# Kernel tuning notes

Hardware: AMD Instinct MI355X
Metric: run time of the kernel (lower is better)

The kernel has to match this reference:

```python
import jax, jax.numpy as jnp
from jax import lax
import numpy as np

V, E, H = 32000, 256, 256  # vocab, embed_dim, rnn_cell_size
B, S = 64, 2048


def setup_inputs() -> dict:
    key = jax.random.key(0)
    ks = jax.random.split(key, 8)
    inv_sqrt_h = 1.0 / np.sqrt(H)
    return {
        "text_inputs": jax.random.randint(ks[0], (B, S), 0, V),
        "mask_input": jnp.ones((B, S), jnp.float32),
        "len_seq": jax.random.randint(ks[1], (B,), 1, S),
        "embed": jax.random.normal(ks[2], (V, E), jnp.float32) * 0.1,
        "W_ih": jax.random.uniform(ks[3], (4 * H, E), jnp.float32, -inv_sqrt_h, inv_sqrt_h),
        "W_hh": jax.random.uniform(ks[4], (4 * H, H), jnp.float32, -inv_sqrt_h, inv_sqrt_h),
        "b_ih": jax.random.uniform(ks[5], (4 * H,), jnp.float32, -inv_sqrt_h, inv_sqrt_h),
        "b_hh": jax.random.uniform(ks[6], (4 * H,), jnp.float32, -inv_sqrt_h, inv_sqrt_h),
    }


def _lstm(x_bse, W_ih, W_hh, b_ih, b_hh):
    # Precompute input contribution in one big GEMM: [B,S,4H]
    pre = jnp.einsum('bse,ge->bsg', x_bse, W_ih) + b_ih
    pre = pre.transpose(1, 0, 2)  # [S,B,4H] for scan over time
    b = x_bse.shape[0]
    h0 = jnp.zeros((b, H), x_bse.dtype)

    def step(carry, p_t):
        h, c = carry
        gates = p_t + h @ W_hh.T + b_hh  # [B,4H], PyTorch gate order i,f,g,o
        i, f, g, o = jnp.split(gates, 4, axis=-1)
        c = jax.nn.sigmoid(f) * c + jax.nn.sigmoid(i) * jnp.tanh(g)
        h = jax.nn.sigmoid(o) * jnp.tanh(c)
        return (h, c), h

    _, hs = lax.scan(step, (h0, h0), pre)  # hs: [S,B,H]
    return hs.transpose(1, 0, 2)  # [B,S,H]


def reference(text_inputs, mask_input, len_seq, embed, W_ih, W_hh, b_ih, b_hh):
    # embedded_dropout with dropout=0 -> plain embedding lookup
    x = embed[text_inputs]  # [B,S,E]
    # sort by length descending (module sorts but never packs)
    order = jnp.argsort(-len_seq)
    x_sorted = x[order]
    out = _lstm(x_sorted, W_ih, W_hh, b_ih, b_hh)
    # LockedDropout inactive in eval -> identity
    inv = jnp.argsort(order)
    out = out[inv]
    return out * mask_input[..., None]
```

## Files before the change

kernel.cpp:

```cpp
#include <hip/hip_runtime.h>

#define S_LEN 2048

typedef _Float16 f16;
typedef _Float16 f16x8 __attribute__((ext_vector_type(8)));
typedef float f32x4 __attribute__((ext_vector_type(4)));

__device__ __forceinline__ float sigf(float x) {
  x = fminf(fmaxf(x, -30.f), 30.f);
  float e = __builtin_amdgcn_exp2f(-1.44269504089f * x);
  return __builtin_amdgcn_rcpf(1.f + e);
}
__device__ __forceinline__ float tanh_fast(float x) {
  x = fminf(fmaxf(x, -15.f), 15.f);
  float e = __builtin_amdgcn_exp2f(2.88539008178f * x);
  return 1.f - 2.f * __builtin_amdgcn_rcpf(e + 1.f);
}

__device__ __forceinline__ void st_hx(unsigned* p, unsigned v) {
  __hip_atomic_store(p, v, __ATOMIC_RELAXED, __HIP_MEMORY_SCOPE_AGENT);
}
__device__ __forceinline__ unsigned ld_hx(const unsigned* p) {
  return __hip_atomic_load(p, __ATOMIC_RELAXED, __HIP_MEMORY_SCOPE_AGENT);
}
__device__ __forceinline__ float swz8(float v) {
  int i = __builtin_bit_cast(int, v);
  int r = __builtin_amdgcn_ds_swizzle(i, 0x201F);
  return __builtin_bit_cast(float, r);
}

__global__ void convert_k(const float* __restrict__ Wih, const float* __restrict__ Whh,
                          const float* __restrict__ bih, const float* __restrict__ bhh,
                          f16* __restrict__ W16, float* __restrict__ bias,
                          unsigned* __restrict__ hx) {
  int i = blockIdx.x * blockDim.x + threadIdx.x;
  int n = i >> 9, k = i & 511;
  W16[i] = (f16)((k < 256) ? Whh[n * 256 + k] : Wih[n * 256 + (k - 256)]);
  if (i < 1024) bias[i] = bih[i] + bhh[i];
  if (i < 32768) hx[i] = 0u;
}

__global__ __launch_bounds__(256, 1) void lstm_k(
    const f16* __restrict__ W16, const float* __restrict__ bias,
    const int* __restrict__ text, const float* __restrict__ embed,
    const float* __restrict__ mask, float* __restrict__ out,
    unsigned* __restrict__ hx) {
  __shared__ __align__(16) f16 h_sw[2][16 * 256];
  __shared__ __align__(16) f16 x_sw[4][16 * 256];

  const int tid = threadIdx.x;
  const int g = blockIdx.x & 7;
  const int slice = blockIdx.x >> 3;
  const int b0 = g * 8;
  const int j0 = slice * 32;

  const int wv = tid >> 6;
  const int l = tid & 63;
  const int kg = l >> 4;
  const int c16 = l & 15;
  const int asw = (c16 & 7) << 3;
  const int gsel = c16 >> 3;
  const int jloc = wv * 8 + (c16 & 7);
  const int jg = j0 + jloc;

  const int r = tid >> 5;
  const int jl = tid & 31;
  const int rsw = (r & 7) << 3;
  const int pd = jl * 8;

  {
    f16x8 z = {(f16)0.f, (f16)0.f, (f16)0.f, (f16)0.f,
               (f16)0.f, (f16)0.f, (f16)0.f, (f16)0.f};
    *(f16x8*)&h_sw[0][tid * 16] = z;
    *(f16x8*)&h_sw[0][tid * 16 + 8] = z;
    *(f16x8*)&h_sw[1][tid * 16] = z;
    *(f16x8*)&h_sw[1][tid * 16 + 8] = z;
  }

  const float bi = bias[0 * 256 + jg];
  const float bf = bias[1 * 256 + jg];
  const float bg = bias[2 * 256 + jg];
  const float bo = bias[3 * 256 + jg];

  f16x8 barr0[16], barr1[16];
  {
    const f16* w0 = W16 + (size_t)(gsel * 256 + jg) * 512 + kg * 8;
    const f16* w1 = W16 + (size_t)((2 + gsel) * 256 + jg) * 512 + kg * 8;
#pragma unroll
    for (int kc = 0; kc < 16; kc++) {
      barr0[kc] = *(const f16x8*)(w0 + kc * 32);
      barr1[kc] = *(const f16x8*)(w1 + kc * 32);
    }
  }

  const int upd = (kg < 2);
  const int bA = kg * 4 + gsel * 2;
  const int bB = bA + 1;
  const int bAc = upd ? bA : 0;
  const int bBc = upd ? bB : 0;
  float ccA = 0.f, ccB = 0.f;

  const size_t trow = (size_t)(b0 + r) * S_LEN;
#pragma unroll 1
  for (int pf = 0; pf < 4; pf++) {
    int idx = text[trow + pf];
    const float4* ep = (const float4*)(embed + (size_t)idx * 256 + pd);
    float4 v0 = ep[0], v1 = ep[1];
    f16x8 hv = {(f16)v0.x, (f16)v0.y, (f16)v0.z, (f16)v0.w,
                (f16)v1.x, (f16)v1.y, (f16)v1.z, (f16)v1.w};
    *(f16x8*)&x_sw[pf][(r * 256 + pd) ^ rsw] = hv;
  }
  float4 rxa, rxb;
  int idx_r;
  {
    int idx4 = text[trow + 4];
    const float4* ep = (const float4*)(embed + (size_t)idx4 * 256 + pd);
    rxa = ep[0];
    rxb = ep[1];
    idx_r = text[trow + 5];
  }

  int offs[7];
#pragma unroll
  for (int p = 0; p < 7; p++) {
    int ps = p + (p >= slice);
    offs[p] = (g * 8 + ps) * 256 + r * 32 + jl;
  }
  const int own_off = (g * 8 + slice) * 256 + bAc * 32 + jloc;

  float mA = mask[(size_t)(b0 + bAc) * S_LEN];
  float mB = mask[(size_t)(b0 + bBc) * S_LEN];

  __syncthreads();

  f32x4 xacc0 = {0.f, 0.f, 0.f, 0.f}, xacc1 = {0.f, 0.f, 0.f, 0.f};
#pragma unroll
  for (int kc = 0; kc < 8; kc++) {
    f16x8 a = *(const f16x8*)&x_sw[0][(c16 * 256 + kc * 32 + kg * 8) ^ asw];
    xacc0 = __builtin_amdgcn_mfma_f32_16x16x32_f16(a, barr0[8 + kc], xacc0, 0, 0, 0);
    xacc1 = __builtin_amdgcn_mfma_f32_16x16x32_f16(a, barr1[8 + kc], xacc1, 0, 0, 0);
  }

  for (int t = 0; t < S_LEN; t++) {
    const f16* hs = h_sw[t & 1];
    f32x4 acc0 = xacc0, acc1 = xacc1;
#pragma unroll
    for (int kc = 0; kc < 8; kc++) {
      f16x8 a = *(const f16x8*)&hs[(c16 * 256 + kc * 32 + kg * 8) ^ asw];
      acc0 = __builtin_amdgcn_mfma_f32_16x16x32_f16(a, barr0[kc], acc0, 0, 0, 0);
      acc1 = __builtin_amdgcn_mfma_f32_16x16x32_f16(a, barr1[kc], acc1, 0, 0, 0);
    }

    float o0_0 = swz8(acc0[0]), o0_1 = swz8(acc0[1]), o0_2 = swz8(acc0[2]), o0_3 = swz8(acc0[3]);
    float o1_0 = swz8(acc1[0]), o1_1 = swz8(acc1[1]), o1_2 = swz8(acc1[2]), o1_3 = swz8(acc1[3]);

    float a0A = gsel ? acc0[2] : acc0[0], a1A = gsel ? acc1[2] : acc1[0];
    float x0A = gsel ? o0_2 : o0_0, x1A = gsel ? o1_2 : o1_0;
    float a0B = gsel ? acc0[3] : acc0[1], a1B = gsel ? acc1[3] : acc1[1];
    float x0B = gsel ? o0_3 : o0_1, x1B = gsel ? o1_3 : o1_1;

    float giA = (gsel ? x0A : a0A) + bi, gfA = (gsel ? a0A : x0A) + bf;
    float ggA = (gsel ? x1A : a1A) + bg, goA = (gsel ? a1A : x1A) + bo;
    float giB = (gsel ? x0B : a0B) + bi, gfB = (gsel ? a0B : x0B) + bf;
    float ggB = (gsel ? x1B : a1B) + bg, goB = (gsel ? a1B : x1B) + bo;

    ccA = sigf(gfA) * ccA + sigf(giA) * tanh_fast(ggA);
    float hA = sigf(goA) * tanh_fast(ccA);
    ccB = sigf(gfB) * ccB + sigf(giB) * tanh_fast(ggB);
    float hB = sigf(goB) * tanh_fast(ccB);

    const int par = (t + 1) & 1;
    unsigned* hb = hx + par * 16384;
    f16* hd = h_sw[par];

    if (upd) {
      unsigned wA = ((unsigned)(t + 1) << 16) |
                    (unsigned)__builtin_bit_cast(unsigned short, (f16)hA);
      unsigned wB = ((unsigned)(t + 1) << 16) |
                    (unsigned)__builtin_bit_cast(unsigned short, (f16)hB);
      st_hx(hb + own_off, wA);
      st_hx(hb + own_off + 32, wB);
      out[((size_t)(b0 + bA) * S_LEN + t) * 256 + jg] = hA * mA;
      out[((size_t)(b0 + bB) * S_LEN + t) * 256 + jg] = hB * mB;
      hd[(bA * 256 + jg) ^ ((bA & 7) << 3)] = (f16)hA;
      hd[(bB * 256 + jg) ^ ((bB & 7) << 3)] = (f16)hB;
    }

    if (t + 1 < S_LEN) {
      mA = mask[(size_t)(b0 + bAc) * S_LEN + (t + 1)];
      mB = mask[(size_t)(b0 + bBc) * S_LEN + (t + 1)];

      const f16* xs = x_sw[(t + 1) & 3];
      f32x4 nx0 = {0.f, 0.f, 0.f, 0.f}, nx1 = {0.f, 0.f, 0.f, 0.f};
#pragma unroll
      for (int kc = 0; kc < 8; kc++) {
        f16x8 a = *(const f16x8*)&xs[(c16 * 256 + kc * 32 + kg * 8) ^ asw];
        nx0 = __builtin_amdgcn_mfma_f32_16x16x32_f16(a, barr0[8 + kc], nx0, 0, 0, 0);
        nx1 = __builtin_amdgcn_mfma_f32_16x16x32_f16(a, barr1[8 + kc], nx1, 0, 0, 0);
      }
      xacc0 = nx0;
      xacc1 = nx1;

      if (t + 4 < S_LEN) {
        f16x8 hv = {(f16)rxa.x, (f16)rxa.y, (f16)rxa.z, (f16)rxa.w,
                    (f16)rxb.x, (f16)rxb.y, (f16)rxb.z, (f16)rxb.w};
        *(f16x8*)&x_sw[t & 3][(r * 256 + pd) ^ rsw] = hv;
      }
      if (t + 5 < S_LEN) {
        const float4* ep = (const float4*)(embed + (size_t)idx_r * 256 + pd);
        rxa = ep[0];
        rxb = ep[1];
      }
      if (t + 6 < S_LEN) idx_r = text[trow + t + 6];

      const unsigned expv = (unsigned)(t + 1);
      unsigned need = 0x7fu;
      unsigned vals[7];
      do {
#pragma unroll
        for (int p = 0; p < 7; p++)
          if (need & (1u << p)) vals[p] = ld_hx(hb + offs[p]);
#pragma unroll
        for (int p = 0; p < 7; p++)
          if ((need & (1u << p)) && (vals[p] >> 16) == expv) need &= ~(1u << p);
      } while (need);
#pragma unroll
      for (int p = 0; p < 7; p++) {
        int ps = p + (p >= slice);
        hd[(r * 256 + ps * 32 + jl) ^ rsw] =
            __builtin_bit_cast(f16, (unsigned short)(vals[p] & 0xffffu));
      }
    }
    __syncthreads();
  }
}

extern "C" void kernel_launch(void* const* d_in, const int* in_sizes, int n_in,
                              void* d_out, int out_size, void* d_ws, size_t ws_size,
                              hipStream_t stream) {
  const int* text = (const int*)d_in[0];
  const float* mask = (const float*)d_in[1];
  const float* embed = (const float*)d_in[3];
  const float* Wih = (const float*)d_in[4];
  const float* Whh = (const float*)d_in[5];
  const float* bih = (const float*)d_in[6];
  const float* bhh = (const float*)d_in[7];
  float* out = (float*)d_out;

  char* ws = (char*)d_ws;
  f16* W16 = (f16*)ws;
  float* bias = (float*)(ws + 1048576);
  unsigned* hx = (unsigned*)(ws + 1052672);

  convert_k<<<2048, 256, 0, stream>>>(Wih, Whh, bih, bhh, W16, bias, hx);
  lstm_k<<<64, 256, 0, stream>>>(W16, bias, text, embed, mask, out, hx);
}
```

Before: 2.980 ms.

## Poll tagged hidden state directly into MFMA fragments, halving blocks to 32

The kernel now runs 32 blocks, each covering 16 batch rows and a 32-column slice, instead of 64 blocks covering 8 rows. The shared-memory h buffer is removed: each wave polls the tagged global hx buffer with 64-bit loads and packs the fp16 halves into MFMA A-fragments with perm instructions. A wave-wide __all on the minimum tag decides readiness. The x-projection is double-buffered two steps ahead, and all lanes now publish. This cuts LDS round trips and one barrier per step. In exchange every wave redundantly polls the full h from global/L2, and fewer blocks use fewer CUs.

New measurement: 10.28 ms. 245% more time.

```diff
diff --git a/kernel.cpp b/kernel.cpp
--- a/kernel.cpp
+++ b/kernel.cpp
@@ -5,6 +5,11 @@
 typedef _Float16 f16;
 typedef _Float16 f16x8 __attribute__((ext_vector_type(8)));
 typedef float f32x4 __attribute__((ext_vector_type(4)));
+typedef unsigned u32;
+typedef unsigned long long u64;
+typedef unsigned u32x4v __attribute__((ext_vector_type(4)));
+
+#define PERM_SEL 0x05040100u
 
 __device__ __forceinline__ float sigf(float x) {
   x = fminf(fmaxf(x, -30.f), 30.f);
@@ -16,23 +21,22 @@
   float e = __builtin_amdgcn_exp2f(2.88539008178f * x);
   return 1.f - 2.f * __builtin_amdgcn_rcpf(e + 1.f);
 }
-
-__device__ __forceinline__ void st_hx(unsigned* p, unsigned v) {
+__device__ __forceinline__ void st_hx(u32* p, u32 v) {
   __hip_atomic_store(p, v, __ATOMIC_RELAXED, __HIP_MEMORY_SCOPE_AGENT);
 }
-__device__ __forceinline__ unsigned ld_hx(const unsigned* p) {
+__device__ __forceinline__ u64 ld_hx64(const u64* p) {
   return __hip_atomic_load(p, __ATOMIC_RELAXED, __HIP_MEMORY_SCOPE_AGENT);
 }
 __device__ __forceinline__ float swz8(float v) {
-  int i = __builtin_bit_cast(int, v);
-  int r = __builtin_amdgcn_ds_swizzle(i, 0x201F);
+  int r = __builtin_amdgcn_ds_swizzle(__builtin_bit_cast(int, v), 0x201F);
   return __builtin_bit_cast(float, r);
 }
+__device__ __forceinline__ u32 umin2(u32 a, u32 b) { return a < b ? a : b; }
 
 __global__ void convert_k(const float* __restrict__ Wih, const float* __restrict__ Whh,
                           const float* __restrict__ bih, const float* __restrict__ bhh,
                           f16* __restrict__ W16, float* __restrict__ bias,
-                          unsigned* __restrict__ hx) {
+                          u32* __restrict__ hx) {
   int i = blockIdx.x * blockDim.x + threadIdx.x;
   int n = i >> 9, k = i & 511;
   W16[i] = (f16)((k < 256) ? Whh[n * 256 + k] : Wih[n * 256 + (k - 256)]);
@@ -44,44 +48,38 @@
     const f16* __restrict__ W16, const float* __restrict__ bias,
     const int* __restrict__ text, const float* __restrict__ embed,
     const float* __restrict__ mask, float* __restrict__ out,
-    unsigned* __restrict__ hx) {
-  __shared__ __align__(16) f16 h_sw[2][16 * 256];
+    u32* __restrict__ hx) {
   __shared__ __align__(16) f16 x_sw[4][16 * 256];
 
   const int tid = threadIdx.x;
-  const int g = blockIdx.x & 7;
-  const int slice = blockIdx.x >> 3;
-  const int b0 = g * 8;
+  const int g = blockIdx.x & 3;
+  const int slice = blockIdx.x >> 2;
+  const int b0 = g * 16;
   const int j0 = slice * 32;
 
   const int wv = tid >> 6;
   const int l = tid & 63;
   const int kg = l >> 4;
   const int c16 = l & 15;
-  const int asw = (c16 & 7) << 3;
   const int gsel = c16 >> 3;
-  const int jloc = wv * 8 + (c16 & 7);
+  const int d3 = c16 & 7;
+  const int jloc = wv * 8 + d3;
   const int jg = j0 + jloc;
-
-  const int r = tid >> 5;
-  const int jl = tid & 31;
-  const int rsw = (r & 7) << 3;
-  const int pd = jl * 8;
-
-  {
-    f16x8 z = {(f16)0.f, (f16)0.f, (f16)0.f, (f16)0.f,
-               (f16)0.f, (f16)0.f, (f16)0.f, (f16)0.f};
-    *(f16x8*)&h_sw[0][tid * 16] = z;
-    *(f16x8*)&h_sw[0][tid * 16 + 8] = z;
-    *(f16x8*)&h_sw[1][tid * 16] = z;
-    *(f16x8*)&h_sw[1][tid * 16 + 8] = z;
-  }
+  const int asw = d3 << 3;
+
+  const int r2 = tid >> 4;
+  const int pd2 = (tid & 15) * 16;
+  const int rsw2 = (r2 & 7) << 3;
 
   const float bi = bias[0 * 256 + jg];
   const float bf = bias[1 * 256 + jg];
   const float bg = bias[2 * 256 + jg];
   const float bo = bias[3 * 256 + jg];
 
+  const int batchA = kg * 4 + gsel * 2;
+  const int batchB = batchA + 1;
+  float ccA = 0.f, ccB = 0.f;
+
   f16x8 barr0[16], barr1[16];
   {
     const f16* w0 = W16 + (size_t)(gsel * 256 + jg) * 512 + kg * 8;
@@ -93,146 +91,142 @@
     }
   }
 
-  const int upd = (kg < 2);
-  const int bA = kg * 4 + gsel * 2;
-  const int bB = bA + 1;
-  const int bAc = upd ? bA : 0;
-  const int bBc = upd ? bB : 0;
-  float ccA = 0.f, ccB = 0.f;
-
-  const size_t trow = (size_t)(b0 + r) * S_LEN;
+  const size_t trow2 = (size_t)(b0 + r2) * S_LEN;
 #pragma unroll 1
   for (int pf = 0; pf < 4; pf++) {
-    int idx = text[trow + pf];
-    const float4* ep = (const float4*)(embed + (size_t)idx * 256 + pd);
-    float4 v0 = ep[0], v1 = ep[1];
-    f16x8 hv = {(f16)v0.x, (f16)v0.y, (f16)v0.z, (f16)v0.w,
+    int idx = text[trow2 + pf];
+    const float4* ep = (const float4*)(embed + (size_t)idx * 256 + pd2);
+    float4 v0 = ep[0], v1 = ep[1], v2 = ep[2], v3 = ep[3];
+    f16x8 h0 = {(f16)v0.x, (f16)v0.y, (f16)v0.z, (f16)v0.w,
                 (f16)v1.x, (f16)v1.y, (f16)v1.z, (f16)v1.w};
-    *(f16x8*)&x_sw[pf][(r * 256 + pd) ^ rsw] = hv;
-  }
-  float4 rxa, rxb;
+    f16x8 h1 = {(f16)v2.x, (f16)v2.y, (f16)v2.z, (f16)v2.w,
+                (f16)v3.x, (f16)v3.y, (f16)v3.z, (f16)v3.w};
+    *(f16x8*)&x_sw[pf][(r2 * 256 + pd2) ^ rsw2] = h0;
+    *(f16x8*)&x_sw[pf][(r2 * 256 + pd2 + 8) ^ rsw2] = h1;
+  }
+  float4 rxa, rxb, rxc, rxd;
   int idx_r;
   {
-    int idx4 = text[trow + 4];
-    const float4* ep = (const float4*)(embed + (size_t)idx4 * 256 + pd);
-    rxa = ep[0];
-    rxb = ep[1];
-    idx_r = text[trow + 5];
-  }
-
-  int offs[7];
-#pragma unroll
-  for (int p = 0; p < 7; p++) {
-    int ps = p + (p >= slice);
-    offs[p] = (g * 8 + ps) * 256 + r * 32 + jl;
-  }
-  const int own_off = (g * 8 + slice) * 256 + bAc * 32 + jloc;
-
-  float mA = mask[(size_t)(b0 + bAc) * S_LEN];
-  float mB = mask[(size_t)(b0 + bBc) * S_LEN];
-
+    int idx4 = text[trow2 + 4];
+    const float4* ep = (const float4*)(embed + (size_t)idx4 * 256 + pd2);
+    rxa = ep[0]; rxb = ep[1]; rxc = ep[2]; rxd = ep[3];
+    idx_r = text[trow2 + 5];
+  }
+  float mA = mask[(size_t)(b0 + batchA) * S_LEN];
+  float mB = mask[(size_t)(b0 + batchB) * S_LEN];
   __syncthreads();
 
-  f32x4 xacc0 = {0.f, 0.f, 0.f, 0.f}, xacc1 = {0.f, 0.f, 0.f, 0.f};
-#pragma unroll
-  for (int kc = 0; kc < 8; kc++) {
-    f16x8 a = *(const f16x8*)&x_sw[0][(c16 * 256 + kc * 32 + kg * 8) ^ asw];
-    xacc0 = __builtin_amdgcn_mfma_f32_16x16x32_f16(a, barr0[8 + kc], xacc0, 0, 0, 0);
-    xacc1 = __builtin_amdgcn_mfma_f32_16x16x32_f16(a, barr1[8 + kc], xacc1, 0, 0, 0);
-  }
-
-  for (int t = 0; t < S_LEN; t++) {
-    const f16* hs = h_sw[t & 1];
-    f32x4 acc0 = xacc0, acc1 = xacc1;
+  auto xpart = [&](int tt, f32x4& X0, f32x4& X1) {
+    const f16* xs = &x_sw[tt & 3][0];
+    f32x4 a0 = {0.f, 0.f, 0.f, 0.f}, a1 = {0.f, 0.f, 0.f, 0.f};
 #pragma unroll
     for (int kc = 0; kc < 8; kc++) {
-      f16x8 a = *(const f16x8*)&hs[(c16 * 256 + kc * 32 + kg * 8) ^ asw];
-      acc0 = __builtin_amdgcn_mfma_f32_16x16x32_f16(a, barr0[kc], acc0, 0, 0, 0);
-      acc1 = __builtin_amdgcn_mfma_f32_16x16x32_f16(a, barr1[kc], acc1, 0, 0, 0);
-    }
-
-    float o0_0 = swz8(acc0[0]), o0_1 = swz8(acc0[1]), o0_2 = swz8(acc0[2]), o0_3 = swz8(acc0[3]);
-    float o1_0 = swz8(acc1[0]), o1_1 = swz8(acc1[1]), o1_2 = swz8(acc1[2]), o1_3 = swz8(acc1[3]);
-
-    float a0A = gsel ? acc0[2] : acc0[0], a1A = gsel ? acc1[2] : acc1[0];
-    float x0A = gsel ? o0_2 : o0_0, x1A = gsel ? o1_2 : o1_0;
-    float a0B = gsel ? acc0[3] : acc0[1], a1B = gsel ? acc1[3] : acc1[1];
-    float x0B = gsel ? o0_3 : o0_1, x1B = gsel ? o1_3 : o1_1;
-
-    float giA = (gsel ? x0A : a0A) + bi, gfA = (gsel ? a0A : x0A) + bf;
-    float ggA = (gsel ? x1A : a1A) + bg, goA = (gsel ? a1A : x1A) + bo;
-    float giB = (gsel ? x0B : a0B) + bi, gfB = (gsel ? a0B : x0B) + bf;
-    float ggB = (gsel ? x1B : a1B) + bg, goB = (gsel ? a1B : x1B) + bo;
+      f16x8 a = *(const f16x8*)&xs[(c16 * 256 + kc * 32 + kg * 8) ^ asw];
+      a0 = __builtin_amdgcn_mfma_f32_16x16x32_f16(a, barr0[8 + kc], a0, 0, 0, 0);
+      a1 = __builtin_amdgcn_mfma_f32_16x16x32_f16(a, barr1[8 + kc], a1, 0, 0, 0);
+    }
+    X0 = a0; X1 = a1;
+  };
+
+  f32x4 XA0, XA1, XB0, XB1;
+  xpart(0, XA0, XA1);
+  xpart(1, XB0, XB1);
+
+  const size_t puboff = (size_t)((g * 8 + slice) * 512 + batchA * 32 + jloc);
+  const size_t pollbase = (size_t)(g * 8) * 256 + (size_t)(c16 * 16 + kg * 4);
+
+  auto step = [&](int t, f32x4& X0, f32x4& X1, bool dopoll) {
+    f32x4 acc0 = X0, acc1 = X1;
+    if (dopoll) {
+      const u32 expv = (u32)t;
+      const u64* hb = (const u64*)hx + (size_t)(t & 1) * 8192 + pollbase;
+      f16x8 frag[8];
+      while (true) {
+        u32 kmn[8];
+#pragma unroll
+        for (int kc = 0; kc < 8; kc++) {
+          u64 v0 = ld_hx64(hb + kc * 256 + 0);
+          u64 v1 = ld_hx64(hb + kc * 256 + 1);
+          u64 v2 = ld_hx64(hb + kc * 256 + 2);
+          u64 v3 = ld_hx64(hb + kc * 256 + 3);
+          u32 w0 = (u32)v0, w1 = (u32)(v0 >> 32);
+          u32 w2 = (u32)v1, w3 = (u32)(v1 >> 32);
+          u32 w4 = (u32)v2, w5 = (u32)(v2 >> 32);
+          u32 w6 = (u32)v3, w7 = (u32)(v3 >> 32);
+          kmn[kc] = umin2(umin2(umin2(w0, w1), umin2(w2, w3)),
+                          umin2(umin2(w4, w5), umin2(w6, w7)));
+          u32x4v u;
+          u.x = __builtin_amdgcn_perm(w1, w0, PERM_SEL);
+          u.y = __builtin_amdgcn_perm(w3, w2, PERM_SEL);
+          u.z = __builtin_amdgcn_perm(w5, w4, PERM_SEL);
+          u.w = __builtin_amdgcn_perm(w7, w6, PERM_SEL);
+          frag[kc] = __builtin_bit_cast(f16x8, u);
+        }
+        u32 mn = umin2(umin2(umin2(kmn[0], kmn[1]), umin2(kmn[2], kmn[3])),
+                       umin2(umin2(kmn[4], kmn[5]), umin2(kmn[6], kmn[7])));
+        if (__all((int)((mn >> 16) == expv))) break;
+      }
+#pragma unroll
+      for (int kc = 0; kc < 8; kc++) {
+        acc0 = __builtin_amdgcn_mfma_f32_16x16x32_f16(frag[kc], barr0[kc], acc0, 0, 0, 0);
+        acc1 = __builtin_amdgcn_mfma_f32_16x16x32_f16(frag[kc], barr1[kc], acc1, 0, 0, 0);
+      }
+    }
+
+    float a0_0 = acc0[0], a0_1 = acc0[1], a0_2 = acc0[2], a0_3 = acc0[3];
+    float a1_0 = acc1[0], a1_1 = acc1[1], a1_2 = acc1[2], a1_3 = acc1[3];
+    float o0_0 = swz8(a0_0), o0_1 = swz8(a0_1), o0_2 = swz8(a0_2), o0_3 = swz8(a0_3);
+    float o1_0 = swz8(a1_0), o1_1 = swz8(a1_1), o1_2 = swz8(a1_2), o1_3 = swz8(a1_3);
+
+    float giA = (gsel ? o0_2 : a0_0) + bi;
+    float gfA = (gsel ? a0_2 : o0_0) + bf;
+    float ggA = (gsel ? o1_2 : a1_0) + bg;
+    float goA = (gsel ? a1_2 : o1_0) + bo;
+    float giB = (gsel ? o0_3 : a0_1) + bi;
+    float gfB = (gsel ? a0_3 : o0_1) + bf;
+    float ggB = (gsel ? o1_3 : a1_1) + bg;
+    float goB = (gsel ? a1_3 : o1_1) + bo;
 
     ccA = sigf(gfA) * ccA + sigf(giA) * tanh_fast(ggA);
     float hA = sigf(goA) * tanh_fast(ccA);
     ccB = sigf(gfB) * ccB + sigf(giB) * tanh_fast(ggB);
     float hB = sigf(goB) * tanh_fast(ccB);
 
-    const int par = (t + 1) & 1;
-    unsigned* hb = hx + par * 16384;
-    f16* hd = h_sw[par];
-
-    if (upd) {
-      unsigned wA = ((unsigned)(t + 1) << 16) |
-                    (unsigned)__builtin_bit_cast(unsigned short, (f16)hA);
-      unsigned wB = ((unsigned)(t + 1) << 16) |
-                    (unsigned)__builtin_bit_cast(unsigned short, (f16)hB);
-      st_hx(hb + own_off, wA);
-      st_hx(hb + own_off + 32, wB);
-      out[((size_t)(b0 + bA) * S_LEN + t) * 256 + jg] = hA * mA;
-      out[((size_t)(b0 + bB) * S_LEN + t) * 256 + jg] = hB * mB;
-      hd[(bA * 256 + jg) ^ ((bA & 7) << 3)] = (f16)hA;
-      hd[(bB * 256 + jg) ^ ((bB & 7) << 3)] = (f16)hB;
-    }
+    const u32 tagv = (u32)(t + 1);
+    u32* hbp = hx + (size_t)((t + 1) & 1) * 16384 + puboff;
+    st_hx(hbp, (tagv << 16) | (u32)__builtin_bit_cast(unsigned short, (f16)hA));
+    st_hx(hbp + 32, (tagv << 16) | (u32)__builtin_bit_cast(unsigned short, (f16)hB));
+    out[((size_t)(b0 + batchA) * S_LEN + t) * 256 + jg] = hA * mA;
+    out[((size_t)(b0 + batchB) * S_LEN + t) * 256 + jg] = hB * mB;
+
+    __syncthreads();
 
     if (t + 1 < S_LEN) {
-      mA = mask[(size_t)(b0 + bAc) * S_LEN + (t + 1)];
-      mB = mask[(size_t)(b0 + bBc) * S_LEN + (t + 1)];
-
-      const f16* xs = x_sw[(t + 1) & 3];
-      f32x4 nx0 = {0.f, 0.f, 0.f, 0.f}, nx1 = {0.f, 0.f, 0.f, 0.f};
-#pragma unroll
-      for (int kc = 0; kc < 8; kc++) {
-        f16x8 a = *(const f16x8*)&xs[(c16 * 256 + kc * 32 + kg * 8) ^ asw];
-        nx0 = __builtin_amdgcn_mfma_f32_16x16x32_f16(a, barr0[8 + kc], nx0, 0, 0, 0);
-        nx1 = __builtin_amdgcn_mfma_f32_16x16x32_f16(a, barr1[8 + kc], nx1, 0, 0, 0);
-      }
-      xacc0 = nx0;
-      xacc1 = nx1;
-
-      if (t + 4 < S_LEN) {
-        f16x8 hv = {(f16)rxa.x, (f16)rxa.y, (f16)rxa.z, (f16)rxa.w,
-                    (f16)rxb.x, (f16)rxb.y, (f16)rxb.z, (f16)rxb.w};
-        *(f16x8*)&x_sw[t & 3][(r * 256 + pd) ^ rsw] = hv;
-      }
-      if (t + 5 < S_LEN) {
-        const float4* ep = (const float4*)(embed + (size_t)idx_r * 256 + pd);
-        rxa = ep[0];
-        rxb = ep[1];
-      }
-      if (t + 6 < S_LEN) idx_r = text[trow + t + 6];
-
-      const unsigned expv = (unsigned)(t + 1);
-      unsigned need = 0x7fu;
-      unsigned vals[7];
-      do {
-#pragma unroll
-        for (int p = 0; p < 7; p++)
-          if (need & (1u << p)) vals[p] = ld_hx(hb + offs[p]);
-#pragma unroll
-        for (int p = 0; p < 7; p++)
-          if ((need & (1u << p)) && (vals[p] >> 16) == expv) need &= ~(1u << p);
-      } while (need);
-#pragma unroll
-      for (int p = 0; p < 7; p++) {
-        int ps = p + (p >= slice);
-        hd[(r * 256 + ps * 32 + jl) ^ rsw] =
-            __builtin_bit_cast(f16, (unsigned short)(vals[p] & 0xffffu));
-      }
-    }
-    __syncthreads();
-  }
+      mA = mask[(size_t)(b0 + batchA) * S_LEN + (t + 1)];
+      mB = mask[(size_t)(b0 + batchB) * S_LEN + (t + 1)];
+    }
+    if (t + 4 < S_LEN) {
+      f16x8 h0 = {(f16)rxa.x, (f16)rxa.y, (f16)rxa.z, (f16)rxa.w,
+                  (f16)rxb.x, (f16)rxb.y, (f16)rxb.z, (f16)rxb.w};
+      f16x8 h1 = {(f16)rxc.x, (f16)rxc.y, (f16)rxc.z, (f16)rxc.w,
+                  (f16)rxd.x, (f16)rxd.y, (f16)rxd.z, (f16)rxd.w};
+      *(f16x8*)&x_sw[t & 3][(r2 * 256 + pd2) ^ rsw2] = h0;
+      *(f16x8*)&x_sw[t & 3][(r2 * 256 + pd2 + 8) ^ rsw2] = h1;
+    }
+    if (t + 5 < S_LEN) {
+      const float4* ep = (const float4*)(embed + (size_t)idx_r * 256 + pd2);
+      rxa = ep[0]; rxb = ep[1]; rxc = ep[2]; rxd = ep[3];
+    }
+    if (t + 6 < S_LEN) idx_r = text[trow2 + t + 6];
+    if (t + 2 < S_LEN) xpart(t + 2, X0, X1);
+  };
+
+  step(0, XA0, XA1, false);
+  for (int t = 1; t + 1 < S_LEN; t += 2) {
+    step(t, XB0, XB1, true);
+    step(t + 1, XA0, XA1, true);
+  }
+  step(S_LEN - 1, XB0, XB1, true);
 }
 
 extern "C" void kernel_launch(void* const* d_in, const int* in_sizes, int n_in,
@@ -250,8 +244,8 @@
   char* ws = (char*)d_ws;
   f16* W16 = (f16*)ws;
   float* bias = (float*)(ws + 1048576);
-  unsigned* hx = (unsigned*)(ws + 1052672);
+  u32* hx = (u32*)(ws + 1052672);
 
   convert_k<<<2048, 256, 0, stream>>>(Wih, Whh, bih, bhh, W16, bias, hx);
-  lstm_k<<<64, 256, 0, stream>>>(W16, bias, text, embed, mask, out, hx);
-}
+  lstm_k<<<32, 256, 0, stream>>>(W16, bias, text, embed, mask, out, hx);
+}
```

## Issue peer h loads before input MFMA, pack stores, and wave-wide poll

Applied to the files above, without the earlier changes.

Changes the cross-block hidden-state exchange. The mailbox layout becomes [j][b], so the two batch values a thread owns go out in one 64-bit atomic store. The first round of peer loads is issued before the next step's input-projection MFMAs, so load latency overlaps the matrix work. The per-slot need-mask spin is replaced by a min-reduction over tags with a wave-wide __all check, and the gate swizzle now uses four ds_swizzle calls instead of eight. The risk is that the min-tag check depends on tag monotonicity, and the wave-wide poll reloads every slot on each retry.

Result: slower. 4.033 ms (+35.3%).

```diff
diff --git a/kernel.cpp b/kernel.cpp
--- a/kernel.cpp
+++ b/kernel.cpp
@@ -5,6 +5,8 @@
 typedef _Float16 f16;
 typedef _Float16 f16x8 __attribute__((ext_vector_type(8)));
 typedef float f32x4 __attribute__((ext_vector_type(4)));
+typedef unsigned u32;
+typedef unsigned long long u64;
 
 __device__ __forceinline__ float sigf(float x) {
   x = fminf(fmaxf(x, -30.f), 30.f);
@@ -16,23 +18,21 @@
   float e = __builtin_amdgcn_exp2f(2.88539008178f * x);
   return 1.f - 2.f * __builtin_amdgcn_rcpf(e + 1.f);
 }
-
-__device__ __forceinline__ void st_hx(unsigned* p, unsigned v) {
+__device__ __forceinline__ void st_hx64(u64* p, u64 v) {
   __hip_atomic_store(p, v, __ATOMIC_RELAXED, __HIP_MEMORY_SCOPE_AGENT);
 }
-__device__ __forceinline__ unsigned ld_hx(const unsigned* p) {
+__device__ __forceinline__ u32 ld_hx(const u32* p) {
   return __hip_atomic_load(p, __ATOMIC_RELAXED, __HIP_MEMORY_SCOPE_AGENT);
 }
 __device__ __forceinline__ float swz8(float v) {
-  int i = __builtin_bit_cast(int, v);
-  int r = __builtin_amdgcn_ds_swizzle(i, 0x201F);
+  int r = __builtin_amdgcn_ds_swizzle(__builtin_bit_cast(int, v), 0x201F);
   return __builtin_bit_cast(float, r);
 }
 
 __global__ void convert_k(const float* __restrict__ Wih, const float* __restrict__ Whh,
                           const float* __restrict__ bih, const float* __restrict__ bhh,
                           f16* __restrict__ W16, float* __restrict__ bias,
-                          unsigned* __restrict__ hx) {
+                          u32* __restrict__ hx) {
   int i = blockIdx.x * blockDim.x + threadIdx.x;
   int n = i >> 9, k = i & 511;
   W16[i] = (f16)((k < 256) ? Whh[n * 256 + k] : Wih[n * 256 + (k - 256)]);
@@ -44,7 +44,7 @@
     const f16* __restrict__ W16, const float* __restrict__ bias,
     const int* __restrict__ text, const float* __restrict__ embed,
     const float* __restrict__ mask, float* __restrict__ out,
-    unsigned* __restrict__ hx) {
+    u32* __restrict__ hx) {
   __shared__ __align__(16) f16 h_sw[2][16 * 256];
   __shared__ __align__(16) f16 x_sw[4][16 * 256];
 
@@ -124,9 +124,9 @@
 #pragma unroll
   for (int p = 0; p < 7; p++) {
     int ps = p + (p >= slice);
-    offs[p] = (g * 8 + ps) * 256 + r * 32 + jl;
-  }
-  const int own_off = (g * 8 + slice) * 256 + bAc * 32 + jloc;
+    offs[p] = (g * 8 + ps) * 256 + jl * 8 + r;
+  }
+  const int pub_idx = ((g * 8 + slice) * 256 + jloc * 8 + bAc) >> 1;
 
   float mA = mask[(size_t)(b0 + bAc) * S_LEN];
   float mB = mask[(size_t)(b0 + bBc) * S_LEN];
@@ -151,18 +151,20 @@
       acc1 = __builtin_amdgcn_mfma_f32_16x16x32_f16(a, barr1[kc], acc1, 0, 0, 0);
     }
 
-    float o0_0 = swz8(acc0[0]), o0_1 = swz8(acc0[1]), o0_2 = swz8(acc0[2]), o0_3 = swz8(acc0[3]);
-    float o1_0 = swz8(acc1[0]), o1_1 = swz8(acc1[1]), o1_2 = swz8(acc1[2]), o1_3 = swz8(acc1[3]);
-
-    float a0A = gsel ? acc0[2] : acc0[0], a1A = gsel ? acc1[2] : acc1[0];
-    float x0A = gsel ? o0_2 : o0_0, x1A = gsel ? o1_2 : o1_0;
-    float a0B = gsel ? acc0[3] : acc0[1], a1B = gsel ? acc1[3] : acc1[1];
-    float x0B = gsel ? o0_3 : o0_1, x1B = gsel ? o1_3 : o1_1;
-
-    float giA = (gsel ? x0A : a0A) + bi, gfA = (gsel ? a0A : x0A) + bf;
-    float ggA = (gsel ? x1A : a1A) + bg, goA = (gsel ? a1A : x1A) + bo;
-    float giB = (gsel ? x0B : a0B) + bi, gfB = (gsel ? a0B : x0B) + bf;
-    float ggB = (gsel ? x1B : a1B) + bg, goB = (gsel ? a1B : x1B) + bo;
+    float s0a = gsel ? acc0[0] : acc0[2];
+    float s0b = gsel ? acc0[1] : acc0[3];
+    float s1a = gsel ? acc1[0] : acc1[2];
+    float s1b = gsel ? acc1[1] : acc1[3];
+    float r0a = swz8(s0a), r0b = swz8(s0b), r1a = swz8(s1a), r1b = swz8(s1b);
+
+    float giA = (gsel ? r0a : acc0[0]) + bi;
+    float gfA = (gsel ? acc0[2] : r0a) + bf;
+    float ggA = (gsel ? r1a : acc1[0]) + bg;
+    float goA = (gsel ? acc1[2] : r1a) + bo;
+    float giB = (gsel ? r0b : acc0[1]) + bi;
+    float gfB = (gsel ? acc0[3] : r0b) + bf;
+    float ggB = (gsel ? r1b : acc1[1]) + bg;
+    float goB = (gsel ? acc1[3] : r1b) + bo;
 
     ccA = sigf(gfA) * ccA + sigf(giA) * tanh_fast(ggA);
     float hA = sigf(goA) * tanh_fast(ccA);
@@ -170,16 +172,14 @@
     float hB = sigf(goB) * tanh_fast(ccB);
 
     const int par = (t + 1) & 1;
-    unsigned* hb = hx + par * 16384;
+    u32* hb32 = hx + (size_t)par * 16384;
     f16* hd = h_sw[par];
+    const u32 tagv = (u32)(t + 1);
 
     if (upd) {
-      unsigned wA = ((unsigned)(t + 1) << 16) |
-                    (unsigned)__builtin_bit_cast(unsigned short, (f16)hA);
-      unsigned wB = ((unsigned)(t + 1) << 16) |
-                    (unsigned)__builtin_bit_cast(unsigned short, (f16)hB);
-      st_hx(hb + own_off, wA);
-      st_hx(hb + own_off + 32, wB);
+      u32 wA = (tagv << 16) | (u32)__builtin_bit_cast(unsigned short, (f16)hA);
+      u32 wB = (tagv << 16) | (u32)__builtin_bit_cast(unsigned short, (f16)hB);
+      st_hx64((u64*)hb32 + pub_idx, ((u64)wB << 32) | wA);
       out[((size_t)(b0 + bA) * S_LEN + t) * 256 + jg] = hA * mA;
       out[((size_t)(b0 + bB) * S_LEN + t) * 256 + jg] = hB * mB;
       hd[(bA * 256 + jg) ^ ((bA & 7) << 3)] = (f16)hA;
@@ -189,18 +189,6 @@
     if (t + 1 < S_LEN) {
       mA = mask[(size_t)(b0 + bAc) * S_LEN + (t + 1)];
       mB = mask[(size_t)(b0 + bBc) * S_LEN + (t + 1)];
-
-      const f16* xs = x_sw[(t + 1) & 3];
-      f32x4 nx0 = {0.f, 0.f, 0.f, 0.f}, nx1 = {0.f, 0.f, 0.f, 0.f};
-#pragma unroll
-      for (int kc = 0; kc < 8; kc++) {
-        f16x8 a = *(const f16x8*)&xs[(c16 * 256 + kc * 32 + kg * 8) ^ asw];
-        nx0 = __builtin_amdgcn_mfma_f32_16x16x32_f16(a, barr0[8 + kc], nx0, 0, 0, 0);
-        nx1 = __builtin_amdgcn_mfma_f32_16x16x32_f16(a, barr1[8 + kc], nx1, 0, 0, 0);
-      }
-      xacc0 = nx0;
-      xacc1 = nx1;
-
       if (t + 4 < S_LEN) {
         f16x8 hv = {(f16)rxa.x, (f16)rxa.y, (f16)rxa.z, (f16)rxa.w,
                     (f16)rxb.x, (f16)rxb.y, (f16)rxb.z, (f16)rxb.w};
@@ -213,22 +201,55 @@
       }
       if (t + 6 < S_LEN) idx_r = text[trow + t + 6];
 
-      const unsigned expv = (unsigned)(t + 1);
-      unsigned need = 0x7fu;
-      unsigned vals[7];
-      do {
-#pragma unroll
-        for (int p = 0; p < 7; p++)
-          if (need & (1u << p)) vals[p] = ld_hx(hb + offs[p]);
-#pragma unroll
-        for (int p = 0; p < 7; p++)
-          if ((need & (1u << p)) && (vals[p] >> 16) == expv) need &= ~(1u << p);
-      } while (need);
-#pragma unroll
-      for (int p = 0; p < 7; p++) {
-        int ps = p + (p >= slice);
-        hd[(r * 256 + ps * 32 + jl) ^ rsw] =
-            __builtin_bit_cast(f16, (unsigned short)(vals[p] & 0xffffu));
+      u32 v0 = ld_hx(hb32 + offs[0]);
+      u32 v1 = ld_hx(hb32 + offs[1]);
+      u32 v2 = ld_hx(hb32 + offs[2]);
+      u32 v3 = ld_hx(hb32 + offs[3]);
+      u32 v4 = ld_hx(hb32 + offs[4]);
+      u32 v5 = ld_hx(hb32 + offs[5]);
+      u32 v6 = ld_hx(hb32 + offs[6]);
+
+      {
+        const f16* xs = x_sw[(t + 1) & 3];
+        f32x4 nx0 = {0.f, 0.f, 0.f, 0.f}, nx1 = {0.f, 0.f, 0.f, 0.f};
+#pragma unroll
+        for (int kc = 0; kc < 8; kc++) {
+          f16x8 a = *(const f16x8*)&xs[(c16 * 256 + kc * 32 + kg * 8) ^ asw];
+          nx0 = __builtin_amdgcn_mfma_f32_16x16x32_f16(a, barr0[8 + kc], nx0, 0, 0, 0);
+          nx1 = __builtin_amdgcn_mfma_f32_16x16x32_f16(a, barr1[8 + kc], nx1, 0, 0, 0);
+        }
+        xacc0 = nx0;
+        xacc1 = nx1;
+      }
+
+      while (true) {
+        u32 m01 = (v0 < v1) ? v0 : v1;
+        u32 m23 = (v2 < v3) ? v2 : v3;
+        u32 m45 = (v4 < v5) ? v4 : v5;
+        u32 m0123 = (m01 < m23) ? m01 : m23;
+        u32 m456 = (m45 < v6) ? m45 : v6;
+        u32 mn = (m0123 < m456) ? m0123 : m456;
+        if (__all((int)((mn >> 16) == tagv))) break;
+        v0 = ld_hx(hb32 + offs[0]);
+        v1 = ld_hx(hb32 + offs[1]);
+        v2 = ld_hx(hb32 + offs[2]);
+        v3 = ld_hx(hb32 + offs[3]);
+        v4 = ld_hx(hb32 + offs[4]);
+        v5 = ld_hx(hb32 + offs[5]);
+        v6 = ld_hx(hb32 + offs[6]);
+      }
+
+      {
+        int ps0 = 0 + (0 >= slice), ps1 = 1 + (1 >= slice), ps2 = 2 + (2 >= slice);
+        int ps3 = 3 + (3 >= slice), ps4 = 4 + (4 >= slice), ps5 = 5 + (5 >= slice);
+        int ps6 = 6 + (6 >= slice);
+        hd[(r * 256 + ps0 * 32 + jl) ^ rsw] = __builtin_bit_cast(f16, (unsigned short)(v0 & 0xffffu));
+        hd[(r * 256 + ps1 * 32 + jl) ^ rsw] = __builtin_bit_cast(f16, (unsigned short)(v1 & 0xffffu));
+        hd[(r * 256 + ps2 * 32 + jl) ^ rsw] = __builtin_bit_cast(f16, (unsigned short)(v2 & 0xffffu));
+        hd[(r * 256 + ps3 * 32 + jl) ^ rsw] = __builtin_bit_cast(f16, (unsigned short)(v3 & 0xffffu));
+        hd[(r * 256 + ps4 * 32 + jl) ^ rsw] = __builtin_bit_cast(f16, (unsigned short)(v4 & 0xffffu));
+        hd[(r * 256 + ps5 * 32 + jl) ^ rsw] = __builtin_bit_cast(f16, (unsigned short)(v5 & 0xffffu));
+        hd[(r * 256 + ps6 * 32 + jl) ^ rsw] = __builtin_bit_cast(f16, (unsigned short)(v6 & 0xffffu));
       }
     }
     __syncthreads();
@@ -250,7 +271,7 @@
   char* ws = (char*)d_ws;
   f16* W16 = (f16*)ws;
   float* bias = (float*)(ws + 1048576);
-  unsigned* hx = (unsigned*)(ws + 1052672);
+  u32* hx = (u32*)(ws + 1052672);
 
   convert_k<<<2048, 256, 0, stream>>>(Wih, Whh, bih, bhh, W16, bias, hx);
   lstm_k<<<64, 256, 0, stream>>>(W16, bias, text, embed, mask, out, hx);
```
